# Kernel tuning notes

Measured on AMD Instinct MI355X. Metric: run time of the kernel, lower is better.

Reference implementation:

```python
import jax, jax.numpy as jnp
import numpy as np

NUM_CLASSES = 10
CLS_W, L1_W, GIOU_W = 2.0, 5.0, 2.0


def box_cxcywh_to_xyxy(b):
    cx, cy, w, h = b[..., 0], b[..., 1], b[..., 2], b[..., 3]
    return jnp.stack([cx - w / 2, cy - h / 2, cx + w / 2, cy + h / 2], axis=-1)


def giou_matrix(b1, b2):
    # b1: (B,N,4), b2: (B,M,4) xyxy -> (B,N,M)
    a1 = jnp.clip(b1[..., 2] - b1[..., 0], 0) * jnp.clip(b1[..., 3] - b1[..., 1], 0)
    a2 = jnp.clip(b2[..., 2] - b2[..., 0], 0) * jnp.clip(b2[..., 3] - b2[..., 1], 0)
    lt = jnp.maximum(b1[..., :, None, :2], b2[..., None, :, :2])
    rb = jnp.minimum(b1[..., :, None, 2:], b2[..., None, :, 2:])
    wh = jnp.clip(rb - lt, 0)
    inter = wh[..., 0] * wh[..., 1]
    union = a1[..., :, None] + a2[..., None, :] - inter
    iou = inter / jnp.clip(union, 1e-6)
    lte = jnp.minimum(b1[..., :, None, :2], b2[..., None, :, :2])
    rbe = jnp.maximum(b1[..., :, None, 2:], b2[..., None, :, 2:])
    whe = jnp.clip(rbe - lte, 0)
    enc = whe[..., 0] * whe[..., 1]
    return iou - (enc - union) / jnp.clip(enc, 1e-6)


def giou_elem(b1, b2):
    # b1, b2: (N,4) xyxy, paired -> (N,)
    a1 = jnp.clip(b1[:, 2] - b1[:, 0], 0) * jnp.clip(b1[:, 3] - b1[:, 1], 0)
    a2 = jnp.clip(b2[:, 2] - b2[:, 0], 0) * jnp.clip(b2[:, 3] - b2[:, 1], 0)
    lt = jnp.maximum(b1[:, :2], b2[:, :2])
    rb = jnp.minimum(b1[:, 2:], b2[:, 2:])
    wh = jnp.clip(rb - lt, 0)
    inter = wh[:, 0] * wh[:, 1]
    union = a1 + a2 - inter
    iou = inter / jnp.clip(union, 1e-6)
    lte = jnp.minimum(b1[:, :2], b2[:, :2])
    rbe = jnp.maximum(b1[:, 2:], b2[:, 2:])
    whe = jnp.clip(rbe - lte, 0)
    enc = whe[:, 0] * whe[:, 1]
    return iou - (enc - union) / jnp.clip(enc, 1e-6)


def hungarian(cost):
    # Jonker-Volgenant style shortest-augmenting-path assignment (== scipy.linear_sum_assignment)
    cost = np.asarray(cost, dtype=np.float64)
    transposed = cost.shape[0] > cost.shape[1]
    C = cost.T if transposed else cost
    n, m = C.shape  # n <= m
    u = np.zeros(n + 1)
    v = np.zeros(m + 1)
    p = np.zeros(m + 1, dtype=np.int64)
    colr = np.arange(m + 1)
    for i in range(1, n + 1):
        p[0] = i
        j0 = 0
        minv = np.full(m + 1, np.inf)
        way = np.zeros(m + 1, dtype=np.int64)
        used = np.zeros(m + 1, dtype=bool)
        while True:
            used[j0] = True
            i0 = p[j0]
            unused = colr[1:][~used[1:]]
            cur = C[i0 - 1, unused - 1] - u[i0] - v[unused]
            better = cur < minv[unused]
            bidx = unused[better]
            minv[bidx] = cur[better]
            way[bidx] = j0
            j1 = unused[np.argmin(minv[unused])]
            delta = minv[j1]
            u[p[used]] += delta
            v[used] -= delta
            minv[~used] -= delta
            j0 = j1
            if p[j0] == 0:
                break
        while j0 != 0:
            jn = way[j0]
            p[j0] = p[jn]
            j0 = jn
    rows = p[1:] - 1
    cols = np.arange(m)
    sel = rows >= 0
    r, c = rows[sel], cols[sel]
    if transposed:
        r, c = c, r
    order = np.argsort(r)
    return r[order], c[order]


def compute_matches(pred_logits, pred_boxes, gt_classes, gt_boxes):
    # Batched cost matrices on device, per-sample Hungarian on host (mirrors torch.no_grad matcher).
    B, Q, _ = pred_logits.shape
    G = gt_classes.shape[1]
    prob = jax.nn.softmax(pred_logits, axis=-1)
    cls_idx = jnp.clip(gt_classes, 0, NUM_CLASSES - 1)
    idx = jnp.broadcast_to(cls_idx[:, None, :], (B, Q, G))
    cls_cost = -jnp.take_along_axis(prob, idx, axis=2)                 # (B,Q,G)
    l1_cost = jnp.abs(pred_boxes[:, :, None, :] - gt_boxes[:, None, :, :]).sum(-1)
    g = giou_matrix(box_cxcywh_to_xyxy(pred_boxes), box_cxcywh_to_xyxy(gt_boxes))
    cost = CLS_W * cls_cost + L1_W * l1_cost - GIOU_W * g
    cost_np = np.asarray(jax.device_get(cost))
    valid_np = np.asarray(jax.device_get(gt_classes)) >= 0
    bs, ps, gs = [], [], []
    for bi in range(B):
        vidx = np.nonzero(valid_np[bi])[0]
        if vidx.size == 0:
            continue
        r, c = hungarian(cost_np[bi][:, vidx])
        bs.append(np.full(r.size, bi, dtype=np.int64))
        ps.append(r.astype(np.int64))
        gs.append(vidx[c].astype(np.int64))
    if bs:
        return np.concatenate(bs), np.concatenate(ps), np.concatenate(gs)
    z = np.zeros(0, np.int64)
    return z, z, z


def detection_loss(pred_logits, pred_boxes, gt_boxes, target_cls, b_f, p_f, g_f, n_matched):
    C1 = pred_logits.shape[-1]
    logp = jax.nn.log_softmax(pred_logits, axis=-1).reshape(-1, C1)
    t = target_cls.reshape(-1)
    w = jnp.ones(C1, dtype=pred_logits.dtype).at[-1].set(0.1)
    nll = -jnp.take_along_axis(logp, t[:, None], axis=1)[:, 0]
    wt = w[t]
    cls_loss = (wt * nll).sum() / wt.sum()
    mp = pred_boxes[b_f, p_f]
    mg = gt_boxes[b_f, g_f]
    l1 = jnp.abs(mp - mg).sum()
    gd = giou_elem(box_cxcywh_to_xyxy(mp), box_cxcywh_to_xyxy(mg))
    gl = (1.0 - gd).sum()
    return CLS_W * cls_loss + L1_W * l1 / n_matched + GIOU_W * gl / n_matched


def setup_inputs() -> dict:
    key = jax.random.key(0)
    k1, k2, k3, k4, k5 = jax.random.split(key, 5)
    B, Q, G, C = 64, 900, 100, NUM_CLASSES
    pred_logits = jax.random.normal(k1, (B, Q, C + 1), dtype=jnp.float32)
    pred_boxes = jax.random.uniform(k2, (B, Q, 4), dtype=jnp.float32, minval=0.05, maxval=0.6)
    gt_boxes = jax.random.uniform(k3, (B, G, 4), dtype=jnp.float32, minval=0.05, maxval=0.6)
    cls = jax.random.randint(k4, (B, G), 0, C)
    nvalid = jax.random.randint(k5, (B,), 1, G + 1)
    mask = jnp.arange(G)[None, :] < nvalid[:, None]
    gt_classes = jnp.where(mask, cls, -1).astype(jnp.int32)
    return {"pred_logits": pred_logits, "pred_boxes": pred_boxes,
            "gt_classes": gt_classes, "gt_boxes": gt_boxes}


def reference(pred_logits, pred_boxes, gt_classes, gt_boxes):
    B, Q = pred_logits.shape[:2]
    b_f, p_f, g_f = compute_matches(pred_logits, pred_boxes, gt_classes, gt_boxes)
    gt_np = np.asarray(jax.device_get(gt_classes))
    tc = np.full((B, Q), NUM_CLASSES, dtype=np.int32)
    tc[b_f, p_f] = gt_np[b_f, g_f]
    n_matched = max(int(b_f.size), 1)
    return detection_loss(pred_logits, pred_boxes, gt_boxes, jnp.asarray(tc), b_f, p_f, g_f, n_matched)
```

## Files before the change

### kernel.cpp

```cpp
#include <hip/hip_runtime.h>
#include <hip/hip_bf16.h>
#include <math.h>

#define BB 64
#define QQ 900
#define GG 100
#define NCLS 10
#define CP1 11

#define STRIDE 960
#define KPL 15
#define NT 512
#define NW 8
#define QMASK 255
#define ROUND_CAP 20000

#define NCH 8
#define QCH 128

#define CLS_W 2.0f
#define L1_W 5.0f
#define GIOU_W 2.0f

struct Accum {
  double wnll, wt, l1, gl;
  int nm, counter;
  int pad[6];
};

__global__ __launch_bounds__(256) void cost_kernel(
    const float* __restrict__ logits, const float* __restrict__ pboxes,
    const int* __restrict__ gcls, const float* __restrict__ gboxes,
    float* __restrict__ cost, float4* __restrict__ part, Accum* acc) {
  const int b = blockIdx.y;
  const int chunk = blockIdx.x;
  const int tid = threadIdx.x;
  const int ql = tid & (QCH - 1);
  const int gh = tid >> 7;
  const int q = chunk * QCH + ql;

  if (chunk == 0 && b == 0 && tid == 0) {
    acc->wnll = 0.0; acc->wt = 0.0; acc->l1 = 0.0; acc->gl = 0.0;
    acc->nm = 0; acc->counter = 0;
  }

  __shared__ float s_gb[GG * 4];
  __shared__ int   s_gc[GG];
  __shared__ float s_prob[QCH * 13];
  __shared__ float s_c[GG][QCH + 1];
  __shared__ float pm1[2][GG], pm2[2][GG];
  __shared__ int   pj1[2][GG];
  __shared__ int   sh_n;

  if (tid == 0) sh_n = 0;
  __syncthreads();

  for (int i = tid; i < GG * 4; i += 256) s_gb[i] = gboxes[b * GG * 4 + i];
  for (int i = tid; i < GG; i += 256) {
    const int v = gcls[b * GG + i];
    s_gc[i] = v;
    if (v >= 0) atomicAdd(&sh_n, 1);
  }

  float pcx = 0.f, pcy = 0.f, pw = 0.f, ph = 0.f;
  if (q < QQ) {
    const float* pb = pboxes + ((size_t)b * QQ + q) * 4;
    pcx = pb[0]; pcy = pb[1]; pw = pb[2]; ph = pb[3];
    if (gh == 0) {
      const float* lg = logits + ((size_t)b * QQ + q) * CP1;
      float l[CP1];
      float mx = -1e30f;
      for (int c = 0; c < CP1; ++c) { l[c] = lg[c]; mx = fmaxf(mx, l[c]); }
      float se = 0.f;
      for (int c = 0; c < CP1; ++c) { l[c] = expf(l[c] - mx); se += l[c]; }
      const float inv = 1.0f / se;
      for (int c = 0; c < NCLS; ++c) s_prob[ql * 13 + c] = l[c] * inv;
    }
  }
  __syncthreads();
  const int sn = sh_n;

  const float px1 = pcx - 0.5f * pw, py1 = pcy - 0.5f * ph;
  const float px2 = pcx + 0.5f * pw, py2 = pcy + 0.5f * ph;
  const float pa = fmaxf(px2 - px1, 0.f) * fmaxf(py2 - py1, 0.f);

  float* crow = cost + ((size_t)b * GG) * STRIDE + q;
  for (int g = gh; g < sn; g += 2) {
    float cv = 3e38f;
    if (q < QQ) {
      int cls = s_gc[g];
      cls = cls < 0 ? 0 : (cls > NCLS - 1 ? NCLS - 1 : cls);
      const float cc = -s_prob[ql * 13 + cls];
      const float gcx = s_gb[g * 4 + 0], gcy = s_gb[g * 4 + 1];
      const float gw  = s_gb[g * 4 + 2], gh2 = s_gb[g * 4 + 3];
      const float l1 = fabsf(pcx - gcx) + fabsf(pcy - gcy) + fabsf(pw - gw) + fabsf(ph - gh2);
      const float gx1 = gcx - 0.5f * gw, gy1 = gcy - 0.5f * gh2;
      const float gx2 = gcx + 0.5f * gw, gy2 = gcy + 0.5f * gh2;
      const float ga = fmaxf(gx2 - gx1, 0.f) * fmaxf(gy2 - gy1, 0.f);
      const float ltx = fmaxf(px1, gx1), lty = fmaxf(py1, gy1);
      const float rbx = fminf(px2, gx2), rby = fminf(py2, gy2);
      const float iw = fmaxf(rbx - ltx, 0.f), ih = fmaxf(rby - lty, 0.f);
      const float inter = iw * ih;
      const float uni = pa + ga - inter;
      const float iou = inter / fmaxf(uni, 1e-6f);
      const float ex1 = fminf(px1, gx1), ey1 = fminf(py1, gy1);
      const float ex2 = fmaxf(px2, gx2), ey2 = fmaxf(py2, gy2);
      const float ew = fmaxf(ex2 - ex1, 0.f), eh = fmaxf(ey2 - ey1, 0.f);
      const float enc = ew * eh;
      const float giou = iou - (enc - uni) / fmaxf(enc, 1e-6f);
      cv = CLS_W * cc + L1_W * l1 - GIOU_W * giou;
      crow[(size_t)g * STRIDE] = cv;
    } else if (q < STRIDE) {
      crow[(size_t)g * STRIDE] = 1e30f;
    }
    s_c[g][ql] = cv;
  }
  __syncthreads();

  {
    const int kmax = (chunk == NCH - 1) ? (QQ - (NCH - 1) * QCH) : QCH;
    const int half = tid >> 7;
    const int r = tid & 127;
    if (r < sn) {
      const int k0 = half ? 64 : 0;
      const int k1 = half ? kmax : (kmax < 64 ? kmax : 64);
      float m1 = 3e38f, m2 = 3e38f;
      int j1 = 0x7FFFFFFF;
      for (int k = k0; k < k1; ++k) {
        const float c = s_c[r][k];
        if (c < m1) { m2 = m1; m1 = c; j1 = 1 + chunk * QCH + k; }
        else if (c < m2) m2 = c;
      }
      pm1[half][r] = m1; pm2[half][r] = m2; pj1[half][r] = j1;
    }
    __syncthreads();
    if (tid < sn) {
      float m1 = pm1[0][tid], m2 = pm2[0][tid];
      int j1 = pj1[0][tid];
      const float n1 = pm1[1][tid], n2 = pm2[1][tid];
      const int i1 = pj1[1][tid];
      if (n1 < m1) { m2 = fminf(m1, n2); m1 = n1; j1 = i1; }
      else m2 = fminf(m2, n1);
      part[((size_t)b * NCH + chunk) * QCH + tid] = make_float4(m1, m2, __int_as_float(j1), 0.f);
    }
  }
}

__global__ __launch_bounds__(NT) void jv_kernel(
    const float* __restrict__ logits, const float* __restrict__ pboxes,
    const int* __restrict__ gcls, const float* __restrict__ gboxes,
    const float* __restrict__ cost, const float4* __restrict__ part,
    Accum* acc, float* out) {
  const int b = blockIdx.x;
  const int tid = threadIdx.x;
  const int lane = tid & 63;
  const int w = tid >> 6;

  __shared__ float vl[STRIDE + 2];
  __shared__ int   p[QQ + 1];
  __shared__ unsigned long long way64[STRIDE + 2];
  __shared__ float m1l[GG + 1], m2l[GG + 1];
  __shared__ int   aminl[GG + 1];
  __shared__ int   s_gc[GG];
  __shared__ int   queue[QMASK + 1];
  __shared__ int   sh_n, sh_qtail, sh_head;
  __shared__ double r0[NW], r1[NW], r2[NW], r3[NW];
  __shared__ int r4[NW];
  __shared__ float s_lse[QQ], s_mx[QQ];

  if (tid == 0) { sh_n = 0; sh_qtail = 0; sh_head = 0; }
  for (int j = tid; j <= QQ; j += NT) p[j] = 0;
  for (int j = tid; j < STRIDE + 2; j += NT) { vl[j] = 0.f; way64[j] = 0ull; }
  if (tid < GG) s_gc[tid] = gcls[b * GG + tid];
  __syncthreads();
  if (tid < GG && s_gc[tid] >= 0) atomicAdd(&sh_n, 1);
  __syncthreads();
  const int n = sh_n;
  const float* Cb = cost + (size_t)b * GG * STRIDE;

  for (int r = tid; r < n; r += NT) {
    float m1 = 3e38f, m2 = 3e38f;
    int j1 = 0x7FFFFFFF;
#pragma unroll
    for (int ch = 0; ch < NCH; ++ch) {
      const float4 pr = part[((size_t)b * NCH + ch) * QCH + r];
      const float pm1 = pr.x, pm2 = pr.y;
      if (pm1 < m1) { m2 = fminf(m1, pm2); m1 = pm1; j1 = __float_as_int(pr.z); }
      else m2 = fminf(m2, pm1);
    }
    m1l[r] = m1; m2l[r] = m2; aminl[r] = j1;
  }
  for (int qq = tid; qq < QQ; qq += NT) {
    const float* lg = logits + ((size_t)b * QQ + qq) * CP1;
    float l[CP1];
    float mx = -1e30f;
    for (int c = 0; c < CP1; ++c) { l[c] = lg[c]; mx = fmaxf(mx, l[c]); }
    float se = 0.f;
    for (int c = 0; c < CP1; ++c) se += expf(l[c] - mx);
    s_mx[qq] = mx;
    s_lse[qq] = logf(se);
  }
  __syncthreads();

  if (tid < n) {
    const float regret = m2l[tid] - m1l[tid];
    const unsigned long long key =
        ((unsigned long long)__float_as_uint(regret) << 20) | (unsigned long long)(tid + 1);
    atomicMax(&way64[aminl[tid]], key);
  }
  __syncthreads();
  if (tid < n) {
    const int j1 = aminl[tid];
    if ((int)(way64[j1] & 0xFFFFFu) == tid + 1) {
      p[j1] = tid + 1;
      vl[j1] = m1l[tid] - m2l[tid];
    } else {
      const int t0 = atomicAdd(&sh_qtail, 1);
      queue[t0 & QMASK] = tid + 1;
    }
  }
  __syncthreads();
  for (int j = tid; j < STRIDE + 2; j += NT) way64[j] = 0ull;
  __syncthreads();

  {
    float pfA[KPL], pfB[KPL];
    int pfAok = 0, pfBok = 0, pfArid = 0, pfBrid = 0;
    int kround = 0;
    while (kround < ROUND_CAP) {
      const int head = sh_head, tail = sh_qtail;
      const int nq = tail - head;
      if (nq <= 0) break;
      const int take = nq < 2 * NW ? nq : 2 * NW;
      ++kround;
      const bool doA = (2 * w < take);
      const bool doB = (2 * w + 1 < take);
      int ridA = 0, ridB = 0;
      float m1A = 3e38f, m2A = 3e38f, m1B = 3e38f, m2B = 3e38f;
      int j1A = 0x7FFFFFFF, j1B = 0x7FFFFFFF;
      if (doA) {
        float rcA[KPL], rcB[KPL];
        if (pfAok) { ridA = pfArid;
#pragma unroll
          for (int k = 0; k < KPL; ++k) rcA[k] = pfA[k];
        } else {
          ridA = queue[(head + 2 * w) & QMASK];
          const float* Cr = Cb + (size_t)(ridA - 1) * STRIDE + lane;
#pragma unroll
          for (int k = 0; k < KPL; ++k) rcA[k] = Cr[k << 6];
        }
        if (doB) {
          if (pfBok) { ridB = pfBrid;
#pragma unroll
            for (int k = 0; k < KPL; ++k) rcB[k] = pfB[k];
          } else {
            ridB = queue[(head + 2 * w + 1) & QMASK];
            const float* Cr = Cb + (size_t)(ridB - 1) * STRIDE + lane;
#pragma unroll
            for (int k = 0; k < KPL; ++k) rcB[k] = Cr[k << 6];
          }
        } else {
#pragma unroll
          for (int k = 0; k < KPL; ++k) rcB[k] = 3e38f;
        }
        float nA1 = 3e38f, nA2 = 3e38f, nB1 = 3e38f, nB2 = 3e38f;
        int iA1 = 0x7FFFFFFF, iB1 = 0x7FFFFFFF;
#pragma unroll
        for (int k = 0; k < 8; ++k) {
          const float vv = vl[1 + lane + (k << 6)];
          const float cA = rcA[k] - vv;
          if (cA < m1A) { m2A = m1A; m1A = cA; j1A = 1 + lane + (k << 6); }
          else if (cA < m2A) m2A = cA;
          const float cB = rcB[k] - vv;
          if (cB < m1B) { m2B = m1B; m1B = cB; j1B = 1 + lane + (k << 6); }
          else if (cB < m2B) m2B = cB;
        }
#pragma unroll
        for (int k = 8; k < KPL; ++k) {
          const float vv = vl[1 + lane + (k << 6)];
          const float cA = rcA[k] - vv;
          if (cA < nA1) { nA2 = nA1; nA1 = cA; iA1 = 1 + lane + (k << 6); }
          else if (cA < nA2) nA2 = cA;
          const float cB = rcB[k] - vv;
          if (cB < nB1) { nB2 = nB1; nB1 = cB; iB1 = 1 + lane + (k << 6); }
          else if (cB < nB2) nB2 = cB;
        }
        if (nA1 < m1A) { m2A = fminf(m1A, nA2); m1A = nA1; j1A = iA1; }
        else m2A = fminf(m2A, nA1);
        if (nB1 < m1B) { m2B = fminf(m1B, nB2); m1B = nB1; j1B = iB1; }
        else m2B = fminf(m2B, nB1);
        for (int m = 1; m < 64; m <<= 1) {
          const float oA1 = __shfl_xor(m1A, m), oA2 = __shfl_xor(m2A, m);
          const int ojA = __shfl_xor(j1A, m);
          const float oB1 = __shfl_xor(m1B, m), oB2 = __shfl_xor(m2B, m);
          const int ojB = __shfl_xor(j1B, m);
          if (oA1 < m1A) { m2A = fminf(m1A, oA2); m1A = oA1; j1A = ojA; }
          else m2A = fminf(m2A, oA1);
          if (oB1 < m1B) { m2B = fminf(m1B, oB2); m1B = oB1; j1B = ojB; }
          else m2B = fminf(m2B, oB1);
        }
        if (lane == 0) {
          float dA = m2A - m1A;
          if (dA < 0.f) dA = 0.f;
          const unsigned long long keyA = ((unsigned long long)kround << 44) |
              ((unsigned long long)__float_as_uint(dA) << 12) | (unsigned long long)ridA;
          atomicMax(&way64[j1A], keyA);
          if (doB) {
            float dB = m2B - m1B;
            if (dB < 0.f) dB = 0.f;
            const unsigned long long keyB = ((unsigned long long)kround << 44) |
                ((unsigned long long)__float_as_uint(dB) << 12) | (unsigned long long)ridB;
            atomicMax(&way64[j1B], keyB);
          }
        }
      }
      pfAok = 0; pfBok = 0;
      {
        const int nh = head + take;
        const int pA = nh + 2 * w, pB = pA + 1;
        if (pA < tail) {
          pfArid = queue[pA & QMASK];
          const float* Cr = Cb + (size_t)(pfArid - 1) * STRIDE + lane;
#pragma unroll
          for (int k = 0; k < KPL; ++k) pfA[k] = Cr[k << 6];
          pfAok = 1;
        }
        if (pB < tail) {
          pfBrid = queue[pB & QMASK];
          const float* Cr = Cb + (size_t)(pfBrid - 1) * STRIDE + lane;
#pragma unroll
          for (int k = 0; k < KPL; ++k) pfB[k] = Cr[k << 6];
          pfBok = 1;
        }
      }
      __syncthreads();
      if (lane == 0 && doA) {
        if ((int)(way64[j1A] & 0xFFFu) == ridA) {
          float dA = m2A - m1A;
          if (dA < 0.f) dA = 0.f;
          const float ov = vl[j1A];
          float nv = ov - dA;
          if (!(nv < ov)) nv = nextafterf(ov, -3e38f);
          vl[j1A] = nv;
          const int k0 = p[j1A];
          p[j1A] = ridA;
          if (k0 > 0) { const int t0 = atomicAdd(&sh_qtail, 1); queue[t0 & QMASK] = k0; }
        } else {
          const int t0 = atomicAdd(&sh_qtail, 1);
          queue[t0 & QMASK] = ridA;
        }
        if (doB) {
          if ((int)(way64[j1B] & 0xFFFu) == ridB) {
            float dB = m2B - m1B;
            if (dB < 0.f) dB = 0.f;
            const float ov = vl[j1B];
            float nv = ov - dB;
            if (!(nv < ov)) nv = nextafterf(ov, -3e38f);
            vl[j1B] = nv;
            const int k0 = p[j1B];
            p[j1B] = ridB;
            if (k0 > 0) { const int t0 = atomicAdd(&sh_qtail, 1); queue[t0 & QMASK] = k0; }
          } else {
            const int t0 = atomicAdd(&sh_qtail, 1);
            queue[t0 & QMASK] = ridB;
          }
        }
      }
      if (tid == 0) sh_head = head + take;
      __syncthreads();
    }
  }
  __syncthreads();

  double wnll = 0.0, wt = 0.0, l1d = 0.0, gld = 0.0;
  int nm = 0;
  for (int q = tid; q < QQ; q += NT) {
    const int idx = b * QQ + q;
    const int g = p[q + 1] - 1;
    const int t = (g >= 0) ? s_gc[g] : NCLS;
    const float lt = logits[(size_t)idx * CP1 + t];
    const float logp = (lt - s_mx[q]) - s_lse[q];
    const float wgt = (t == NCLS) ? 0.1f : 1.0f;
    wnll += (double)(wgt * (-logp));
    wt += (double)wgt;
    if (g >= 0) {
      nm += 1;
      const float* pb = pboxes + (size_t)idx * 4;
      const float* gb = gboxes + ((size_t)b * GG + g) * 4;
      const float pcx = pb[0], pcy = pb[1], pw = pb[2], ph = pb[3];
      const float gcx = gb[0], gcy = gb[1], gw = gb[2], gh = gb[3];
      const float l1 = fabsf(pcx - gcx) + fabsf(pcy - gcy) + fabsf(pw - gw) + fabsf(ph - gh);
      const float px1 = pcx - 0.5f * pw, py1 = pcy - 0.5f * ph;
      const float px2 = pcx + 0.5f * pw, py2 = pcy + 0.5f * ph;
      const float gx1 = gcx - 0.5f * gw, gy1 = gcy - 0.5f * gh;
      const float gx2 = gcx + 0.5f * gw, gy2 = gcy + 0.5f * gh;
      const float pa = fmaxf(px2 - px1, 0.f) * fmaxf(py2 - py1, 0.f);
      const float ga = fmaxf(gx2 - gx1, 0.f) * fmaxf(gy2 - gy1, 0.f);
      const float ltx = fmaxf(px1, gx1), lty = fmaxf(py1, gy1);
      const float rbx = fminf(px2, gx2), rby = fminf(py2, gy2);
      const float iw = fmaxf(rbx - ltx, 0.f), ih = fmaxf(rby - lty, 0.f);
      const float inter = iw * ih;
      const float uni = pa + ga - inter;
      const float iou = inter / fmaxf(uni, 1e-6f);
      const float ex1 = fminf(px1, gx1), ey1 = fminf(py1, gy1);
      const float ex2 = fmaxf(px2, gx2), ey2 = fmaxf(py2, gy2);
      const float ew = fmaxf(ex2 - ex1, 0.f), eh = fmaxf(ey2 - ey1, 0.f);
      const float enc = ew * eh;
      const float giou = iou - (enc - uni) / fmaxf(enc, 1e-6f);
      l1d += (double)l1;
      gld += (double)(1.0f - giou);
    }
  }

  for (int off = 32; off; off >>= 1) {
    wnll += __shfl_down(wnll, off);
    wt   += __shfl_down(wt, off);
    l1d  += __shfl_down(l1d, off);
    gld  += __shfl_down(gld, off);
    nm   += __shfl_down(nm, off);
  }
  if (lane == 0) { r0[w] = wnll; r1[w] = wt; r2[w] = l1d; r3[w] = gld; r4[w] = nm; }
  __syncthreads();
  if (tid == 0) {
    for (int x = 1; x < NW; ++x) { wnll += r0[x]; wt += r1[x]; l1d += r2[x]; gld += r3[x]; nm += r4[x]; }
    atomicAdd(&acc->wnll, wnll);
    atomicAdd(&acc->wt, wt);
    atomicAdd(&acc->l1, l1d);
    atomicAdd(&acc->gl, gld);
    atomicAdd(&acc->nm, nm);
    __threadfence();
    const int ticket = atomicAdd(&acc->counter, 1);
    if (ticket == BB - 1) {
      const double fw = atomicAdd(&acc->wnll, 0.0);
      const double fwt = atomicAdd(&acc->wt, 0.0);
      const double fl1 = atomicAdd(&acc->l1, 0.0);
      const double fgl = atomicAdd(&acc->gl, 0.0);
      int fnm = atomicAdd(&acc->nm, 0);
      if (fnm < 1) fnm = 1;
      const double loss = (double)CLS_W * (fw / fwt) +
                          ((double)L1_W * fl1 + (double)GIOU_W * fgl) / (double)fnm;
      out[0] = (float)loss;
    }
  }
}

extern "C" void kernel_launch(void* const* d_in, const int* in_sizes, int n_in,
                              void* d_out, int out_size, void* d_ws, size_t ws_size,
                              hipStream_t stream) {
  const float* logits = (const float*)d_in[0];
  const float* pboxes = (const float*)d_in[1];
  const int*   gcls   = (const int*)d_in[2];
  const float* gboxes = (const float*)d_in[3];

  char* ws = (char*)d_ws;
  Accum* acc = (Accum*)ws;
  float4* part = (float4*)(ws + 4096);
  float* cost = (float*)(ws + 4096 + (size_t)BB * NCH * QCH * sizeof(float4));

  cost_kernel<<<dim3(NCH, BB), 256, 0, stream>>>(logits, pboxes, gcls, gboxes, cost, part, acc);
  jv_kernel<<<BB, NT, 0, stream>>>(logits, pboxes, gcls, gboxes, cost, part, acc, (float*)d_out);
}
```

Measured before the change: 104.3 us.

## Fuse cost and assignment kernels into one launch with per-batch completion flags

Merges the cost-matrix kernel and the JV assignment kernel into a single launch. The first 256 blocks each compute two query chunks, and the trailing 64 blocks do the assignment per batch item. The assignment blocks run their softmax/LSE setup first, then spin on a per-batch done counter before reading the partial minima. The two phases share one shared-memory union, and the accumulator plus counters are zeroed with a memset. This removes the inter-kernel launch gap and lets early batches start assignment while others still compute cost. The risk is a deadlock if the spinning blocks take residency ahead of the producer blocks, and each cost block now has half its threads idle during softmax.

```diff
diff --git a/kernel.cpp b/kernel.cpp
--- a/kernel.cpp
+++ b/kernel.cpp
@@ -1,5 +1,4 @@
 #include <hip/hip_runtime.h>
-#include <hip/hip_bf16.h>
 #include <math.h>
 
 #define BB 64
@@ -17,6 +16,8 @@
 
 #define NCH 8
 #define QCH 128
+#define CPB 4
+#define CBLK (BB * CPB)
 
 #define CLS_W 2.0f
 #define L1_W 5.0f
@@ -28,168 +29,167 @@
   int pad[6];
 };
 
-__global__ __launch_bounds__(256) void cost_kernel(
+union SharedU {
+  struct {
+    float s_c[GG][QCH + 1];
+    float s_prob[QCH * 13];
+    float s_gb[GG * 4];
+    int   s_gc[GG];
+    float pm1[2][GG], pm2[2][GG];
+    int   pj1[2][GG];
+    int   sh_n;
+  } c;
+  struct {
+    float vl[STRIDE + 2];
+    int   p[QQ + 1];
+    unsigned long long way64[STRIDE + 2];
+    float m1l[GG + 1], m2l[GG + 1];
+    int   aminl[GG + 1];
+    int   s_gc[GG];
+    int   queue[QMASK + 1];
+    int   sh_n, sh_qtail, sh_head;
+    double r0[NW], r1[NW], r2[NW], r3[NW];
+    int   r4[NW];
+    float s_lse[QQ], s_mx[QQ];
+  } j;
+};
+
+__global__ __launch_bounds__(NT) void det_kernel(
     const float* __restrict__ logits, const float* __restrict__ pboxes,
     const int* __restrict__ gcls, const float* __restrict__ gboxes,
-    float* __restrict__ cost, float4* __restrict__ part, Accum* acc) {
-  const int b = blockIdx.y;
-  const int chunk = blockIdx.x;
+    float* __restrict__ cost, float4* __restrict__ part,
+    int* __restrict__ done, Accum* acc, float* out) {
+  __shared__ SharedU su;
   const int tid = threadIdx.x;
-  const int ql = tid & (QCH - 1);
-  const int gh = tid >> 7;
-  const int q = chunk * QCH + ql;
-
-  if (chunk == 0 && b == 0 && tid == 0) {
-    acc->wnll = 0.0; acc->wt = 0.0; acc->l1 = 0.0; acc->gl = 0.0;
-    acc->nm = 0; acc->counter = 0;
-  }
-
-  __shared__ float s_gb[GG * 4];
-  __shared__ int   s_gc[GG];
-  __shared__ float s_prob[QCH * 13];
-  __shared__ float s_c[GG][QCH + 1];
-  __shared__ float pm1[2][GG], pm2[2][GG];
-  __shared__ int   pj1[2][GG];
-  __shared__ int   sh_n;
-
-  if (tid == 0) sh_n = 0;
-  __syncthreads();
-
-  for (int i = tid; i < GG * 4; i += 256) s_gb[i] = gboxes[b * GG * 4 + i];
-  for (int i = tid; i < GG; i += 256) {
-    const int v = gcls[b * GG + i];
-    s_gc[i] = v;
-    if (v >= 0) atomicAdd(&sh_n, 1);
-  }
-
-  float pcx = 0.f, pcy = 0.f, pw = 0.f, ph = 0.f;
-  if (q < QQ) {
-    const float* pb = pboxes + ((size_t)b * QQ + q) * 4;
-    pcx = pb[0]; pcy = pb[1]; pw = pb[2]; ph = pb[3];
-    if (gh == 0) {
-      const float* lg = logits + ((size_t)b * QQ + q) * CP1;
-      float l[CP1];
-      float mx = -1e30f;
-      for (int c = 0; c < CP1; ++c) { l[c] = lg[c]; mx = fmaxf(mx, l[c]); }
-      float se = 0.f;
-      for (int c = 0; c < CP1; ++c) { l[c] = expf(l[c] - mx); se += l[c]; }
-      const float inv = 1.0f / se;
-      for (int c = 0; c < NCLS; ++c) s_prob[ql * 13 + c] = l[c] * inv;
-    }
-  }
-  __syncthreads();
-  const int sn = sh_n;
-
-  const float px1 = pcx - 0.5f * pw, py1 = pcy - 0.5f * ph;
-  const float px2 = pcx + 0.5f * pw, py2 = pcy + 0.5f * ph;
-  const float pa = fmaxf(px2 - px1, 0.f) * fmaxf(py2 - py1, 0.f);
-
-  float* crow = cost + ((size_t)b * GG) * STRIDE + q;
-  for (int g = gh; g < sn; g += 2) {
-    float cv = 3e38f;
-    if (q < QQ) {
-      int cls = s_gc[g];
-      cls = cls < 0 ? 0 : (cls > NCLS - 1 ? NCLS - 1 : cls);
-      const float cc = -s_prob[ql * 13 + cls];
-      const float gcx = s_gb[g * 4 + 0], gcy = s_gb[g * 4 + 1];
-      const float gw  = s_gb[g * 4 + 2], gh2 = s_gb[g * 4 + 3];
-      const float l1 = fabsf(pcx - gcx) + fabsf(pcy - gcy) + fabsf(pw - gw) + fabsf(ph - gh2);
-      const float gx1 = gcx - 0.5f * gw, gy1 = gcy - 0.5f * gh2;
-      const float gx2 = gcx + 0.5f * gw, gy2 = gcy + 0.5f * gh2;
-      const float ga = fmaxf(gx2 - gx1, 0.f) * fmaxf(gy2 - gy1, 0.f);
-      const float ltx = fmaxf(px1, gx1), lty = fmaxf(py1, gy1);
-      const float rbx = fminf(px2, gx2), rby = fminf(py2, gy2);
-      const float iw = fmaxf(rbx - ltx, 0.f), ih = fmaxf(rby - lty, 0.f);
-      const float inter = iw * ih;
-      const float uni = pa + ga - inter;
-      const float iou = inter / fmaxf(uni, 1e-6f);
-      const float ex1 = fminf(px1, gx1), ey1 = fminf(py1, gy1);
-      const float ex2 = fmaxf(px2, gx2), ey2 = fmaxf(py2, gy2);
-      const float ew = fmaxf(ex2 - ex1, 0.f), eh = fmaxf(ey2 - ey1, 0.f);
-      const float enc = ew * eh;
-      const float giou = iou - (enc - uni) / fmaxf(enc, 1e-6f);
-      cv = CLS_W * cc + L1_W * l1 - GIOU_W * giou;
-      crow[(size_t)g * STRIDE] = cv;
-    } else if (q < STRIDE) {
-      crow[(size_t)g * STRIDE] = 1e30f;
-    }
-    s_c[g][ql] = cv;
-  }
-  __syncthreads();
-
-  {
-    const int kmax = (chunk == NCH - 1) ? (QQ - (NCH - 1) * QCH) : QCH;
-    const int half = tid >> 7;
-    const int r = tid & 127;
-    if (r < sn) {
-      const int k0 = half ? 64 : 0;
-      const int k1 = half ? kmax : (kmax < 64 ? kmax : 64);
-      float m1 = 3e38f, m2 = 3e38f;
-      int j1 = 0x7FFFFFFF;
-      for (int k = k0; k < k1; ++k) {
-        const float c = s_c[r][k];
-        if (c < m1) { m2 = m1; m1 = c; j1 = 1 + chunk * QCH + k; }
-        else if (c < m2) m2 = c;
-      }
-      pm1[half][r] = m1; pm2[half][r] = m2; pj1[half][r] = j1;
-    }
+
+  if (blockIdx.x < CBLK) {
+    auto& C = su.c;
+    const int b = blockIdx.x >> 2;
+    const int cpair = blockIdx.x & 3;
+    const int ql = tid & (QCH - 1);
+    const int gq = tid >> 7;
+
+    if (tid == 0) C.sh_n = 0;
     __syncthreads();
-    if (tid < sn) {
-      float m1 = pm1[0][tid], m2 = pm2[0][tid];
-      int j1 = pj1[0][tid];
-      const float n1 = pm1[1][tid], n2 = pm2[1][tid];
-      const int i1 = pj1[1][tid];
-      if (n1 < m1) { m2 = fminf(m1, n2); m1 = n1; j1 = i1; }
-      else m2 = fminf(m2, n1);
-      part[((size_t)b * NCH + chunk) * QCH + tid] = make_float4(m1, m2, __int_as_float(j1), 0.f);
-    }
-  }
-}
-
-__global__ __launch_bounds__(NT) void jv_kernel(
-    const float* __restrict__ logits, const float* __restrict__ pboxes,
-    const int* __restrict__ gcls, const float* __restrict__ gboxes,
-    const float* __restrict__ cost, const float4* __restrict__ part,
-    Accum* acc, float* out) {
-  const int b = blockIdx.x;
-  const int tid = threadIdx.x;
+    for (int i = tid; i < GG * 4; i += NT) C.s_gb[i] = gboxes[b * GG * 4 + i];
+    for (int i = tid; i < GG; i += NT) {
+      const int v = gcls[b * GG + i];
+      C.s_gc[i] = v;
+      if (v >= 0) atomicAdd(&C.sh_n, 1);
+    }
+    __syncthreads();
+    const int sn = C.sh_n;
+
+    for (int half = 0; half < 2; ++half) {
+      const int cc = cpair + half * 4;
+      const int q = cc * QCH + ql;
+
+      if (tid < QCH) {
+        const int qs = cc * QCH + tid;
+        if (qs < QQ) {
+          const float* lg = logits + ((size_t)b * QQ + qs) * CP1;
+          float l[CP1];
+          float mx = -1e30f;
+          for (int c = 0; c < CP1; ++c) { l[c] = lg[c]; mx = fmaxf(mx, l[c]); }
+          float se = 0.f;
+          for (int c = 0; c < CP1; ++c) { l[c] = expf(l[c] - mx); se += l[c]; }
+          const float inv = 1.0f / se;
+          for (int c = 0; c < NCLS; ++c) C.s_prob[tid * 13 + c] = l[c] * inv;
+        }
+      }
+      __syncthreads();
+
+      float pcx = 0.f, pcy = 0.f, pw = 0.f, ph = 0.f;
+      if (q < QQ) {
+        const float* pb = pboxes + ((size_t)b * QQ + q) * 4;
+        pcx = pb[0]; pcy = pb[1]; pw = pb[2]; ph = pb[3];
+      }
+      const float px1 = pcx - 0.5f * pw, py1 = pcy - 0.5f * ph;
+      const float px2 = pcx + 0.5f * pw, py2 = pcy + 0.5f * ph;
+      const float pa = fmaxf(px2 - px1, 0.f) * fmaxf(py2 - py1, 0.f);
+
+      float* crow = cost + ((size_t)b * GG) * STRIDE + q;
+      for (int g = gq; g < sn; g += 4) {
+        float cv = 3e38f;
+        if (q < QQ) {
+          int cls = C.s_gc[g];
+          cls = cls < 0 ? 0 : (cls > NCLS - 1 ? NCLS - 1 : cls);
+          const float ccst = -C.s_prob[ql * 13 + cls];
+          const float gcx = C.s_gb[g * 4 + 0], gcy = C.s_gb[g * 4 + 1];
+          const float gw  = C.s_gb[g * 4 + 2], gh2 = C.s_gb[g * 4 + 3];
+          const float l1 = fabsf(pcx - gcx) + fabsf(pcy - gcy) + fabsf(pw - gw) + fabsf(ph - gh2);
+          const float gx1 = gcx - 0.5f * gw, gy1 = gcy - 0.5f * gh2;
+          const float gx2 = gcx + 0.5f * gw, gy2 = gcy + 0.5f * gh2;
+          const float ga = fmaxf(gx2 - gx1, 0.f) * fmaxf(gy2 - gy1, 0.f);
+          const float ltx = fmaxf(px1, gx1), lty = fmaxf(py1, gy1);
+          const float rbx = fminf(px2, gx2), rby = fminf(py2, gy2);
+          const float iw = fmaxf(rbx - ltx, 0.f), ih = fmaxf(rby - lty, 0.f);
+          const float inter = iw * ih;
+          const float uni = pa + ga - inter;
+          const float iou = inter / fmaxf(uni, 1e-6f);
+          const float ex1 = fminf(px1, gx1), ey1 = fminf(py1, gy1);
+          const float ex2 = fmaxf(px2, gx2), ey2 = fmaxf(py2, gy2);
+          const float ew = fmaxf(ex2 - ex1, 0.f), eh = fmaxf(ey2 - ey1, 0.f);
+          const float enc = ew * eh;
+          const float giou = iou - (enc - uni) / fmaxf(enc, 1e-6f);
+          cv = CLS_W * ccst + L1_W * l1 - GIOU_W * giou;
+          crow[(size_t)g * STRIDE] = cv;
+        } else if (q < STRIDE) {
+          crow[(size_t)g * STRIDE] = 1e30f;
+        }
+        C.s_c[g][ql] = cv;
+      }
+      __syncthreads();
+
+      {
+        const int kmax = (cc == NCH - 1) ? (QQ - (NCH - 1) * QCH) : QCH;
+        if (tid < 256) {
+          const int sh = tid >> 7;
+          const int r = tid & 127;
+          if (r < sn) {
+            const int k0 = sh ? 64 : 0;
+            const int k1 = sh ? kmax : (kmax < 64 ? kmax : 64);
+            float m1 = 3e38f, m2 = 3e38f;
+            int j1 = 0x7FFFFFFF;
+            for (int k = k0; k < k1; ++k) {
+              const float c = C.s_c[r][k];
+              if (c < m1) { m2 = m1; m1 = c; j1 = 1 + cc * QCH + k; }
+              else if (c < m2) m2 = c;
+            }
+            C.pm1[sh][r] = m1; C.pm2[sh][r] = m2; C.pj1[sh][r] = j1;
+          }
+        }
+        __syncthreads();
+        if (tid < sn) {
+          float m1 = C.pm1[0][tid], m2 = C.pm2[0][tid];
+          int j1 = C.pj1[0][tid];
+          const float n1 = C.pm1[1][tid], n2 = C.pm2[1][tid];
+          const int i1 = C.pj1[1][tid];
+          if (n1 < m1) { m2 = fminf(m1, n2); m1 = n1; j1 = i1; }
+          else m2 = fminf(m2, n1);
+          part[((size_t)b * NCH + cc) * QCH + tid] = make_float4(m1, m2, __int_as_float(j1), 0.f);
+        }
+      }
+      __syncthreads();
+      if (tid == 0) {
+        __threadfence();
+        atomicAdd(&done[b], 1);
+      }
+    }
+    return;
+  }
+
+  auto& J = su.j;
+  const int b = blockIdx.x - CBLK;
   const int lane = tid & 63;
   const int w = tid >> 6;
 
-  __shared__ float vl[STRIDE + 2];
-  __shared__ int   p[QQ + 1];
-  __shared__ unsigned long long way64[STRIDE + 2];
-  __shared__ float m1l[GG + 1], m2l[GG + 1];
-  __shared__ int   aminl[GG + 1];
-  __shared__ int   s_gc[GG];
-  __shared__ int   queue[QMASK + 1];
-  __shared__ int   sh_n, sh_qtail, sh_head;
-  __shared__ double r0[NW], r1[NW], r2[NW], r3[NW];
-  __shared__ int r4[NW];
-  __shared__ float s_lse[QQ], s_mx[QQ];
-
-  if (tid == 0) { sh_n = 0; sh_qtail = 0; sh_head = 0; }
-  for (int j = tid; j <= QQ; j += NT) p[j] = 0;
-  for (int j = tid; j < STRIDE + 2; j += NT) { vl[j] = 0.f; way64[j] = 0ull; }
-  if (tid < GG) s_gc[tid] = gcls[b * GG + tid];
-  __syncthreads();
-  if (tid < GG && s_gc[tid] >= 0) atomicAdd(&sh_n, 1);
-  __syncthreads();
-  const int n = sh_n;
-  const float* Cb = cost + (size_t)b * GG * STRIDE;
-
-  for (int r = tid; r < n; r += NT) {
-    float m1 = 3e38f, m2 = 3e38f;
-    int j1 = 0x7FFFFFFF;
-#pragma unroll
-    for (int ch = 0; ch < NCH; ++ch) {
-      const float4 pr = part[((size_t)b * NCH + ch) * QCH + r];
-      const float pm1 = pr.x, pm2 = pr.y;
-      if (pm1 < m1) { m2 = fminf(m1, pm2); m1 = pm1; j1 = __float_as_int(pr.z); }
-      else m2 = fminf(m2, pm1);
-    }
-    m1l[r] = m1; m2l[r] = m2; aminl[r] = j1;
-  }
+  if (tid == 0) { J.sh_n = 0; J.sh_qtail = 0; J.sh_head = 0; }
+  for (int j = tid; j <= QQ; j += NT) J.p[j] = 0;
+  for (int j = tid; j < STRIDE + 2; j += NT) { J.vl[j] = 0.f; J.way64[j] = 0ull; }
+  if (tid < GG) J.s_gc[tid] = gcls[b * GG + tid];
+  __syncthreads();
+  if (tid < GG && J.s_gc[tid] >= 0) atomicAdd(&J.sh_n, 1);
   for (int qq = tid; qq < QQ; qq += NT) {
     const float* lg = logits + ((size_t)b * QQ + qq) * CP1;
     float l[CP1];
@@ -197,30 +197,53 @@
     for (int c = 0; c < CP1; ++c) { l[c] = lg[c]; mx = fmaxf(mx, l[c]); }
     float se = 0.f;
     for (int c = 0; c < CP1; ++c) se += expf(l[c] - mx);
-    s_mx[qq] = mx;
-    s_lse[qq] = logf(se);
+    J.s_mx[qq] = mx;
+    J.s_lse[qq] = logf(se);
+  }
+  __syncthreads();
+  const int n = J.sh_n;
+  const float* Cb = cost + (size_t)b * GG * STRIDE;
+
+  if (tid == 0) {
+    while (__hip_atomic_load(done + b, __ATOMIC_ACQUIRE, __HIP_MEMORY_SCOPE_AGENT) < NCH)
+      __builtin_amdgcn_s_sleep(2);
+  }
+  __syncthreads();
+  __threadfence();
+
+  for (int r = tid; r < n; r += NT) {
+    float m1 = 3e38f, m2 = 3e38f;
+    int j1 = 0x7FFFFFFF;
+#pragma unroll
+    for (int ch = 0; ch < NCH; ++ch) {
+      const float4 pr = part[((size_t)b * NCH + ch) * QCH + r];
+      const float pm1 = pr.x, pm2 = pr.y;
+      if (pm1 < m1) { m2 = fminf(m1, pm2); m1 = pm1; j1 = __float_as_int(pr.z); }
+      else m2 = fminf(m2, pm1);
+    }
+    J.m1l[r] = m1; J.m2l[r] = m2; J.aminl[r] = j1;
   }
   __syncthreads();
 
   if (tid < n) {
-    const float regret = m2l[tid] - m1l[tid];
+    const float regret = J.m2l[tid] - J.m1l[tid];
     const unsigned long long key =
         ((unsigned long long)__float_as_uint(regret) << 20) | (unsigned long long)(tid + 1);
-    atomicMax(&way64[aminl[tid]], key);
+    atomicMax(&J.way64[J.aminl[tid]], key);
   }
   __syncthreads();
   if (tid < n) {
-    const int j1 = aminl[tid];
-    if ((int)(way64[j1] & 0xFFFFFu) == tid + 1) {
-      p[j1] = tid + 1;
-      vl[j1] = m1l[tid] - m2l[tid];
+    const int j1 = J.aminl[tid];
+    if ((int)(J.way64[j1] & 0xFFFFFu) == tid + 1) {
+      J.p[j1] = tid + 1;
+      J.vl[j1] = J.m1l[tid] - J.m2l[tid];
     } else {
-      const int t0 = atomicAdd(&sh_qtail, 1);
-      queue[t0 & QMASK] = tid + 1;
-    }
-  }
-  __syncthreads();
-  for (int j = tid; j < STRIDE + 2; j += NT) way64[j] = 0ull;
+      const int t0 = atomicAdd(&J.sh_qtail, 1);
+      J.queue[t0 & QMASK] = tid + 1;
+    }
+  }
+  __syncthreads();
+  for (int j = tid; j < STRIDE + 2; j += NT) J.way64[j] = 0ull;
   __syncthreads();
 
   {
@@ -228,7 +251,7 @@
     int pfAok = 0, pfBok = 0, pfArid = 0, pfBrid = 0;
     int kround = 0;
     while (kround < ROUND_CAP) {
-      const int head = sh_head, tail = sh_qtail;
+      const int head = J.sh_head, tail = J.sh_qtail;
       const int nq = tail - head;
       if (nq <= 0) break;
       const int take = nq < 2 * NW ? nq : 2 * NW;
@@ -244,7 +267,7 @@
 #pragma unroll
           for (int k = 0; k < KPL; ++k) rcA[k] = pfA[k];
         } else {
-          ridA = queue[(head + 2 * w) & QMASK];
+          ridA = J.queue[(head + 2 * w) & QMASK];
           const float* Cr = Cb + (size_t)(ridA - 1) * STRIDE + lane;
 #pragma unroll
           for (int k = 0; k < KPL; ++k) rcA[k] = Cr[k << 6];
@@ -254,7 +277,7 @@
 #pragma unroll
             for (int k = 0; k < KPL; ++k) rcB[k] = pfB[k];
           } else {
-            ridB = queue[(head + 2 * w + 1) & QMASK];
+            ridB = J.queue[(head + 2 * w + 1) & QMASK];
             const float* Cr = Cb + (size_t)(ridB - 1) * STRIDE + lane;
 #pragma unroll
             for (int k = 0; k < KPL; ++k) rcB[k] = Cr[k << 6];
@@ -267,7 +290,7 @@
         int iA1 = 0x7FFFFFFF, iB1 = 0x7FFFFFFF;
 #pragma unroll
         for (int k = 0; k < 8; ++k) {
-          const float vv = vl[1 + lane + (k << 6)];
+          const float vv = J.vl[1 + lane + (k << 6)];
           const float cA = rcA[k] - vv;
           if (cA < m1A) { m2A = m1A; m1A = cA; j1A = 1 + lane + (k << 6); }
           else if (cA < m2A) m2A = cA;
@@ -277,7 +300,7 @@
         }
 #pragma unroll
         for (int k = 8; k < KPL; ++k) {
-          const float vv = vl[1 + lane + (k << 6)];
+          const float vv = J.vl[1 + lane + (k << 6)];
           const float cA = rcA[k] - vv;
           if (cA < nA1) { nA2 = nA1; nA1 = cA; iA1 = 1 + lane + (k << 6); }
           else if (cA < nA2) nA2 = cA;
@@ -304,13 +327,13 @@
           if (dA < 0.f) dA = 0.f;
           const unsigned long long keyA = ((unsigned long long)kround << 44) |
               ((unsigned long long)__float_as_uint(dA) << 12) | (unsigned long long)ridA;
-          atomicMax(&way64[j1A], keyA);
+          atomicMax(&J.way64[j1A], keyA);
           if (doB) {
             float dB = m2B - m1B;
             if (dB < 0.f) dB = 0.f;
             const unsigned long long keyB = ((unsigned long long)kround << 44) |
                 ((unsigned long long)__float_as_uint(dB) << 12) | (unsigned long long)ridB;
-            atomicMax(&way64[j1B], keyB);
+            atomicMax(&J.way64[j1B], keyB);
           }
         }
       }
@@ -319,14 +342,14 @@
         const int nh = head + take;
         const int pA = nh + 2 * w, pB = pA + 1;
         if (pA < tail) {
-          pfArid = queue[pA & QMASK];
+          pfArid = J.queue[pA & QMASK];
           const float* Cr = Cb + (size_t)(pfArid - 1) * STRIDE + lane;
 #pragma unroll
           for (int k = 0; k < KPL; ++k) pfA[k] = Cr[k << 6];
           pfAok = 1;
         }
         if (pB < tail) {
-          pfBrid = queue[pB & QMASK];
+          pfBrid = J.queue[pB & QMASK];
           const float* Cr = Cb + (size_t)(pfBrid - 1) * STRIDE + lane;
 #pragma unroll
           for (int k = 0; k < KPL; ++k) pfB[k] = Cr[k << 6];
@@ -335,38 +358,38 @@
       }
       __syncthreads();
       if (lane == 0 && doA) {
-        if ((int)(way64[j1A] & 0xFFFu) == ridA) {
+        if ((int)(J.way64[j1A] & 0xFFFu) == ridA) {
           float dA = m2A - m1A;
           if (dA < 0.f) dA = 0.f;
-          const float ov = vl[j1A];
+          const float ov = J.vl[j1A];
           float nv = ov - dA;
           if (!(nv < ov)) nv = nextafterf(ov, -3e38f);
-          vl[j1A] = nv;
-          const int k0 = p[j1A];
-          p[j1A] = ridA;
-          if (k0 > 0) { const int t0 = atomicAdd(&sh_qtail, 1); queue[t0 & QMASK] = k0; }
+          J.vl[j1A] = nv;
+          const int k0 = J.p[j1A];
+          J.p[j1A] = ridA;
+          if (k0 > 0) { const int t0 = atomicAdd(&J.sh_qtail, 1); J.queue[t0 & QMASK] = k0; }
         } else {
-          const int t0 = atomicAdd(&sh_qtail, 1);
-          queue[t0 & QMASK] = ridA;
+          const int t0 = atomicAdd(&J.sh_qtail, 1);
+          J.queue[t0 & QMASK] = ridA;
         }
         if (doB) {
-          if ((int)(way64[j1B] & 0xFFFu) == ridB) {
+          if ((int)(J.way64[j1B] & 0xFFFu) == ridB) {
             float dB = m2B - m1B;
             if (dB < 0.f) dB = 0.f;
-            const float ov = vl[j1B];
+            const float ov = J.vl[j1B];
             float nv = ov - dB;
             if (!(nv < ov)) nv = nextafterf(ov, -3e38f);
-            vl[j1B] = nv;
-            const int k0 = p[j1B];
-            p[j1B] = ridB;
-            if (k0 > 0) { const int t0 = atomicAdd(&sh_qtail, 1); queue[t0 & QMASK] = k0; }
+            J.vl[j1B] = nv;
+            const int k0 = J.p[j1B];
+            J.p[j1B] = ridB;
+            if (k0 > 0) { const int t0 = atomicAdd(&J.sh_qtail, 1); J.queue[t0 & QMASK] = k0; }
           } else {
-            const int t0 = atomicAdd(&sh_qtail, 1);
-            queue[t0 & QMASK] = ridB;
+            const int t0 = atomicAdd(&J.sh_qtail, 1);
+            J.queue[t0 & QMASK] = ridB;
           }
         }
       }
-      if (tid == 0) sh_head = head + take;
+      if (tid == 0) J.sh_head = head + take;
       __syncthreads();
     }
   }
@@ -376,10 +399,10 @@
   int nm = 0;
   for (int q = tid; q < QQ; q += NT) {
     const int idx = b * QQ + q;
-    const int g = p[q + 1] - 1;
-    const int t = (g >= 0) ? s_gc[g] : NCLS;
+    const int g = J.p[q + 1] - 1;
+    const int t = (g >= 0) ? J.s_gc[g] : NCLS;
     const float lt = logits[(size_t)idx * CP1 + t];
-    const float logp = (lt - s_mx[q]) - s_lse[q];
+    const float logp = (lt - J.s_mx[q]) - J.s_lse[q];
     const float wgt = (t == NCLS) ? 0.1f : 1.0f;
     wnll += (double)(wgt * (-logp));
     wt += (double)wgt;
@@ -419,10 +442,10 @@
     gld  += __shfl_down(gld, off);
     nm   += __shfl_down(nm, off);
   }
-  if (lane == 0) { r0[w] = wnll; r1[w] = wt; r2[w] = l1d; r3[w] = gld; r4[w] = nm; }
+  if (lane == 0) { J.r0[w] = wnll; J.r1[w] = wt; J.r2[w] = l1d; J.r3[w] = gld; J.r4[w] = nm; }
   __syncthreads();
   if (tid == 0) {
-    for (int x = 1; x < NW; ++x) { wnll += r0[x]; wt += r1[x]; l1d += r2[x]; gld += r3[x]; nm += r4[x]; }
+    for (int x = 1; x < NW; ++x) { wnll += J.r0[x]; wt += J.r1[x]; l1d += J.r2[x]; gld += J.r3[x]; nm += J.r4[x]; }
     atomicAdd(&acc->wnll, wnll);
     atomicAdd(&acc->wt, wt);
     atomicAdd(&acc->l1, l1d);
@@ -454,9 +477,11 @@
 
   char* ws = (char*)d_ws;
   Accum* acc = (Accum*)ws;
+  int* done = (int*)(ws + 256);
   float4* part = (float4*)(ws + 4096);
   float* cost = (float*)(ws + 4096 + (size_t)BB * NCH * QCH * sizeof(float4));
 
-  cost_kernel<<<dim3(NCH, BB), 256, 0, stream>>>(logits, pboxes, gcls, gboxes, cost, part, acc);
-  jv_kernel<<<BB, NT, 0, stream>>>(logits, pboxes, gcls, gboxes, cost, part, acc, (float*)d_out);
+  hipMemsetAsync(ws, 0, 4096, stream);
+  det_kernel<<<CBLK + BB, NT, 0, stream>>>(logits, pboxes, gcls, gboxes,
+                                           cost, part, done, acc, (float*)d_out);
 }
```

Measured after the change: 124.8 us. +19.7%, slower.

## Run auction assignment loop in a single wavefront with register-resident prices

Applied to the files above, without the earlier changes.

Moves the assignment loop onto wave 0 alone. Column prices live in per-lane registers and the queue head and tail live in registers. This drops both per-round __syncthreads barriers, the shared-memory atomicMax conflict resolution and the shared atomic queue appends. The wave handles up to two rows per round, resolves conflicts between them directly, and raises its scheduling priority. The other waves read the cost rows once to warm the cache. In exchange, far fewer rows are bid on per round, so more rounds are needed, and tie-breaking between conflicting bids changes.

```diff
diff --git a/kernel.cpp b/kernel.cpp
--- a/kernel.cpp
+++ b/kernel.cpp
@@ -163,12 +163,12 @@
   __shared__ int   aminl[GG + 1];
   __shared__ int   s_gc[GG];
   __shared__ int   queue[QMASK + 1];
-  __shared__ int   sh_n, sh_qtail, sh_head;
+  __shared__ int   sh_n, sh_qtail;
   __shared__ double r0[NW], r1[NW], r2[NW], r3[NW];
   __shared__ int r4[NW];
   __shared__ float s_lse[QQ], s_mx[QQ];
 
-  if (tid == 0) { sh_n = 0; sh_qtail = 0; sh_head = 0; }
+  if (tid == 0) { sh_n = 0; sh_qtail = 0; }
   for (int j = tid; j <= QQ; j += NT) p[j] = 0;
   for (int j = tid; j < STRIDE + 2; j += NT) { vl[j] = 0.f; way64[j] = 0ull; }
   if (tid < GG) s_gc[tid] = gcls[b * GG + tid];
@@ -220,154 +220,153 @@
     }
   }
   __syncthreads();
-  for (int j = tid; j < STRIDE + 2; j += NT) way64[j] = 0ull;
-  __syncthreads();
-
-  {
+
+  if (w == 0) {
+    __builtin_amdgcn_s_setprio(1);
+    float v[KPL];
+#pragma unroll
+    for (int k = 0; k < KPL; ++k) v[k] = vl[1 + lane + (k << 6)];
+    int head = 0, tail = sh_qtail, rounds = 0;
+
     float pfA[KPL], pfB[KPL];
-    int pfAok = 0, pfBok = 0, pfArid = 0, pfBrid = 0;
-    int kround = 0;
-    while (kround < ROUND_CAP) {
-      const int head = sh_head, tail = sh_qtail;
+    int pfApos = -1, pfBpos = -1, pfArid = 0, pfBrid = 0;
+
+    while (head < tail && rounds < ROUND_CAP) {
       const int nq = tail - head;
-      if (nq <= 0) break;
-      const int take = nq < 2 * NW ? nq : 2 * NW;
-      ++kround;
-      const bool doA = (2 * w < take);
-      const bool doB = (2 * w + 1 < take);
-      int ridA = 0, ridB = 0;
-      float m1A = 3e38f, m2A = 3e38f, m1B = 3e38f, m2B = 3e38f;
-      int j1A = 0x7FFFFFFF, j1B = 0x7FFFFFFF;
-      if (doA) {
-        float rcA[KPL], rcB[KPL];
-        if (pfAok) { ridA = pfArid;
-#pragma unroll
-          for (int k = 0; k < KPL; ++k) rcA[k] = pfA[k];
+      const int take = nq >= 2 ? 2 : 1;
+      ++rounds;
+
+      int ridA, ridB = 0;
+      float rcA[KPL], rcB[KPL];
+      if (pfApos == head) {
+        ridA = pfArid;
+#pragma unroll
+        for (int k = 0; k < KPL; ++k) rcA[k] = pfA[k];
+      } else {
+        ridA = queue[head & QMASK];
+        const float* Cr = Cb + (size_t)(ridA - 1) * STRIDE + lane;
+#pragma unroll
+        for (int k = 0; k < KPL; ++k) rcA[k] = Cr[k << 6];
+      }
+      if (take == 2) {
+        if (pfBpos == head + 1) {
+          ridB = pfBrid;
+#pragma unroll
+          for (int k = 0; k < KPL; ++k) rcB[k] = pfB[k];
         } else {
-          ridA = queue[(head + 2 * w) & QMASK];
-          const float* Cr = Cb + (size_t)(ridA - 1) * STRIDE + lane;
-#pragma unroll
-          for (int k = 0; k < KPL; ++k) rcA[k] = Cr[k << 6];
+          ridB = queue[(head + 1) & QMASK];
+          const float* Cr = Cb + (size_t)(ridB - 1) * STRIDE + lane;
+#pragma unroll
+          for (int k = 0; k < KPL; ++k) rcB[k] = Cr[k << 6];
         }
-        if (doB) {
-          if (pfBok) { ridB = pfBrid;
-#pragma unroll
-            for (int k = 0; k < KPL; ++k) rcB[k] = pfB[k];
-          } else {
-            ridB = queue[(head + 2 * w + 1) & QMASK];
-            const float* Cr = Cb + (size_t)(ridB - 1) * STRIDE + lane;
-#pragma unroll
-            for (int k = 0; k < KPL; ++k) rcB[k] = Cr[k << 6];
-          }
-        } else {
-#pragma unroll
-          for (int k = 0; k < KPL; ++k) rcB[k] = 3e38f;
-        }
-        float nA1 = 3e38f, nA2 = 3e38f, nB1 = 3e38f, nB2 = 3e38f;
-        int iA1 = 0x7FFFFFFF, iB1 = 0x7FFFFFFF;
-#pragma unroll
-        for (int k = 0; k < 8; ++k) {
-          const float vv = vl[1 + lane + (k << 6)];
-          const float cA = rcA[k] - vv;
-          if (cA < m1A) { m2A = m1A; m1A = cA; j1A = 1 + lane + (k << 6); }
-          else if (cA < m2A) m2A = cA;
-          const float cB = rcB[k] - vv;
-          if (cB < m1B) { m2B = m1B; m1B = cB; j1B = 1 + lane + (k << 6); }
-          else if (cB < m2B) m2B = cB;
-        }
-#pragma unroll
-        for (int k = 8; k < KPL; ++k) {
-          const float vv = vl[1 + lane + (k << 6)];
-          const float cA = rcA[k] - vv;
-          if (cA < nA1) { nA2 = nA1; nA1 = cA; iA1 = 1 + lane + (k << 6); }
-          else if (cA < nA2) nA2 = cA;
-          const float cB = rcB[k] - vv;
-          if (cB < nB1) { nB2 = nB1; nB1 = cB; iB1 = 1 + lane + (k << 6); }
-          else if (cB < nB2) nB2 = cB;
-        }
-        if (nA1 < m1A) { m2A = fminf(m1A, nA2); m1A = nA1; j1A = iA1; }
-        else m2A = fminf(m2A, nA1);
-        if (nB1 < m1B) { m2B = fminf(m1B, nB2); m1B = nB1; j1B = iB1; }
-        else m2B = fminf(m2B, nB1);
-        for (int m = 1; m < 64; m <<= 1) {
-          const float oA1 = __shfl_xor(m1A, m), oA2 = __shfl_xor(m2A, m);
-          const int ojA = __shfl_xor(j1A, m);
-          const float oB1 = __shfl_xor(m1B, m), oB2 = __shfl_xor(m2B, m);
-          const int ojB = __shfl_xor(j1B, m);
-          if (oA1 < m1A) { m2A = fminf(m1A, oA2); m1A = oA1; j1A = ojA; }
-          else m2A = fminf(m2A, oA1);
-          if (oB1 < m1B) { m2B = fminf(m1B, oB2); m1B = oB1; j1B = ojB; }
-          else m2B = fminf(m2B, oB1);
-        }
-        if (lane == 0) {
-          float dA = m2A - m1A;
-          if (dA < 0.f) dA = 0.f;
-          const unsigned long long keyA = ((unsigned long long)kround << 44) |
-              ((unsigned long long)__float_as_uint(dA) << 12) | (unsigned long long)ridA;
-          atomicMax(&way64[j1A], keyA);
-          if (doB) {
-            float dB = m2B - m1B;
-            if (dB < 0.f) dB = 0.f;
-            const unsigned long long keyB = ((unsigned long long)kround << 44) |
-                ((unsigned long long)__float_as_uint(dB) << 12) | (unsigned long long)ridB;
-            atomicMax(&way64[j1B], keyB);
-          }
-        }
-      }
-      pfAok = 0; pfBok = 0;
+      } else {
+#pragma unroll
+        for (int k = 0; k < KPL; ++k) rcB[k] = 3e38f;
+      }
+
+      pfApos = -1; pfBpos = -1;
       {
-        const int nh = head + take;
-        const int pA = nh + 2 * w, pB = pA + 1;
+        const int pA = head + take, pB = head + take + 1;
         if (pA < tail) {
           pfArid = queue[pA & QMASK];
           const float* Cr = Cb + (size_t)(pfArid - 1) * STRIDE + lane;
 #pragma unroll
           for (int k = 0; k < KPL; ++k) pfA[k] = Cr[k << 6];
-          pfAok = 1;
+          pfApos = pA;
         }
         if (pB < tail) {
           pfBrid = queue[pB & QMASK];
           const float* Cr = Cb + (size_t)(pfBrid - 1) * STRIDE + lane;
 #pragma unroll
           for (int k = 0; k < KPL; ++k) pfB[k] = Cr[k << 6];
-          pfBok = 1;
+          pfBpos = pB;
         }
       }
-      __syncthreads();
-      if (lane == 0 && doA) {
-        if ((int)(way64[j1A] & 0xFFFu) == ridA) {
-          float dA = m2A - m1A;
-          if (dA < 0.f) dA = 0.f;
-          const float ov = vl[j1A];
+
+      float m1A = 3e38f, m2A = 3e38f, m1B = 3e38f, m2B = 3e38f;
+      int j1A = 0x7FFFFFFF, j1B = 0x7FFFFFFF;
+      float nA1 = 3e38f, nA2 = 3e38f, nB1 = 3e38f, nB2 = 3e38f;
+      int iA1 = 0x7FFFFFFF, iB1 = 0x7FFFFFFF;
+#pragma unroll
+      for (int k = 0; k < 8; ++k) {
+        const float vv = v[k];
+        const float cA = rcA[k] - vv;
+        if (cA < m1A) { m2A = m1A; m1A = cA; j1A = 1 + lane + (k << 6); }
+        else if (cA < m2A) m2A = cA;
+        const float cB = rcB[k] - vv;
+        if (cB < m1B) { m2B = m1B; m1B = cB; j1B = 1 + lane + (k << 6); }
+        else if (cB < m2B) m2B = cB;
+      }
+#pragma unroll
+      for (int k = 8; k < KPL; ++k) {
+        const float vv = v[k];
+        const float cA = rcA[k] - vv;
+        if (cA < nA1) { nA2 = nA1; nA1 = cA; iA1 = 1 + lane + (k << 6); }
+        else if (cA < nA2) nA2 = cA;
+        const float cB = rcB[k] - vv;
+        if (cB < nB1) { nB2 = nB1; nB1 = cB; iB1 = 1 + lane + (k << 6); }
+        else if (cB < nB2) nB2 = cB;
+      }
+      if (nA1 < m1A) { m2A = fminf(m1A, nA2); m1A = nA1; j1A = iA1; }
+      else m2A = fminf(m2A, nA1);
+      if (nB1 < m1B) { m2B = fminf(m1B, nB2); m1B = nB1; j1B = iB1; }
+      else m2B = fminf(m2B, nB1);
+      for (int m = 1; m < 64; m <<= 1) {
+        const float oA1 = __shfl_xor(m1A, m), oA2 = __shfl_xor(m2A, m);
+        const int ojA = __shfl_xor(j1A, m);
+        const float oB1 = __shfl_xor(m1B, m), oB2 = __shfl_xor(m2B, m);
+        const int ojB = __shfl_xor(j1B, m);
+        if (oA1 < m1A) { m2A = fminf(m1A, oA2); m1A = oA1; j1A = ojA; }
+        else m2A = fminf(m2A, oA1);
+        if (oB1 < m1B) { m2B = fminf(m1B, oB2); m1B = oB1; j1B = ojB; }
+        else m2B = fminf(m2B, oB1);
+      }
+
+      {
+        float dA = m2A - m1A;
+        if (dA < 0.f) dA = 0.f;
+        const int c0 = j1A - 1;
+        if ((c0 & 63) == lane) {
+          const int kk = c0 >> 6;
+          const float ov = v[kk];
           float nv = ov - dA;
           if (!(nv < ov)) nv = nextafterf(ov, -3e38f);
-          vl[j1A] = nv;
-          const int k0 = p[j1A];
-          p[j1A] = ridA;
-          if (k0 > 0) { const int t0 = atomicAdd(&sh_qtail, 1); queue[t0 & QMASK] = k0; }
+          v[kk] = nv;
+        }
+        const int k0 = p[j1A];
+        p[j1A] = ridA;
+        if (k0 > 0) { if (lane == 0) queue[tail & QMASK] = k0; tail++; }
+      }
+      if (take == 2) {
+        if (j1B == j1A) {
+          if (lane == 0) queue[tail & QMASK] = ridB;
+          tail++;
         } else {
-          const int t0 = atomicAdd(&sh_qtail, 1);
-          queue[t0 & QMASK] = ridA;
-        }
-        if (doB) {
-          if ((int)(way64[j1B] & 0xFFFu) == ridB) {
-            float dB = m2B - m1B;
-            if (dB < 0.f) dB = 0.f;
-            const float ov = vl[j1B];
+          float dB = m2B - m1B;
+          if (dB < 0.f) dB = 0.f;
+          const int c0 = j1B - 1;
+          if ((c0 & 63) == lane) {
+            const int kk = c0 >> 6;
+            const float ov = v[kk];
             float nv = ov - dB;
             if (!(nv < ov)) nv = nextafterf(ov, -3e38f);
-            vl[j1B] = nv;
-            const int k0 = p[j1B];
-            p[j1B] = ridB;
-            if (k0 > 0) { const int t0 = atomicAdd(&sh_qtail, 1); queue[t0 & QMASK] = k0; }
-          } else {
-            const int t0 = atomicAdd(&sh_qtail, 1);
-            queue[t0 & QMASK] = ridB;
+            v[kk] = nv;
           }
+          const int k0 = p[j1B];
+          p[j1B] = ridB;
+          if (k0 > 0) { if (lane == 0) queue[tail & QMASK] = k0; tail++; }
         }
       }
-      if (tid == 0) sh_head = head + take;
-      __syncthreads();
+      head += take;
+    }
+    __builtin_amdgcn_s_setprio(0);
+  } else {
+    for (int r = w - 1; r < n; r += NW - 1) {
+      const float* Cr = Cb + (size_t)r * STRIDE + lane;
+      float s = 0.f;
+#pragma unroll
+      for (int k = 0; k < KPL; ++k) s += Cr[k << 6];
+      asm volatile("" :: "v"(s));
     }
   }
   __syncthreads();
```

After: 113.5 us. 1.09x slower.
